# Kernel tuning notes

Hardware: AMD Instinct MI355X
Metric: run time of the kernel (lower is better)

Reference implementation:

```python
import jax, jax.numpy as jnp
import numpy as np

N_NODES = 50000


def gcn_conv(x, W, b, src, dst, n_nodes):
    """PyG GCNConv: h = x @ W; add self-loops; symmetric norm; scatter-add; + bias."""
    h = x @ W  # [N, out]
    loop = jnp.arange(n_nodes, dtype=src.dtype)
    s = jnp.concatenate([src, loop])  # source nodes j
    d = jnp.concatenate([dst, loop])  # target nodes i
    deg = jax.ops.segment_sum(jnp.ones_like(d, dtype=h.dtype), d, num_segments=n_nodes)
    dinv = jnp.where(deg > 0, jax.lax.rsqrt(deg), 0.0)
    norm = dinv[s] * dinv[d]  # [E+N]
    msg = h[s] * norm[:, None]  # gather + scale, [E+N, out]
    out = jax.ops.segment_sum(msg, d, num_segments=n_nodes)
    return out + b


def setup_inputs() -> dict:
    key = jax.random.key(0)
    k1, k2, k3, k4 = jax.random.split(key, 4)
    x = jax.random.normal(k1, (N_NODES, 256), dtype=jnp.float32)
    edge_index = jax.random.randint(k2, (2, 1600000), 0, N_NODES, dtype=jnp.int64)
    in_dim, hid, out_dim = 256, 128, 40
    W1 = jax.random.normal(k3, (in_dim, hid), dtype=jnp.float32) / np.sqrt(in_dim)
    b1 = jnp.zeros((hid,), dtype=jnp.float32)
    W2 = jax.random.normal(k4, (hid, out_dim), dtype=jnp.float32) / np.sqrt(hid)
    b2 = jnp.zeros((out_dim,), dtype=jnp.float32)
    return {"x": x, "edge_index": edge_index, "W1": W1, "b1": b1, "W2": W2, "b2": b2}


def reference(x, edge_index, W1, b1, W2, b2):
    src, dst = edge_index[0], edge_index[1]
    n = x.shape[0]
    h = jax.nn.relu(gcn_conv(x, W1, b1, src, dst, n))
    # dropout is identity in eval mode
    h = gcn_conv(h, W2, b2, src, dst, n)
    return jax.nn.log_softmax(h, axis=1)
```

## Files before the change

kernel.cpp:

```cpp
#include <hip/hip_runtime.h>
#include <cmath>

#define NN 50000
#define C_IN 256
#define C_HID 128
#define C_OUT 40

#define BSZ 512
#define NBUCK ((NN + BSZ - 1) / BSZ)
#define CAP 19456
#define EPB 4096

typedef __attribute__((ext_vector_type(8))) short bf16x8;
typedef __attribute__((ext_vector_type(4))) float f32x4;
typedef __attribute__((ext_vector_type(2))) float f32x2;

__device__ __forceinline__ float bf2f(unsigned int u16) {
  unsigned int b = (u16 & 0xFFFFu) << 16;
  return __builtin_bit_cast(float, b);
}
__device__ __forceinline__ unsigned short f2bf(float f) {
  unsigned int b = __builtin_bit_cast(unsigned int, f);
  unsigned int r = (b + 0x7FFF + ((b >> 16) & 1)) >> 16;
  return (unsigned short)r;
}


__global__ __launch_bounds__(256) void passA_kernel(const int* __restrict__ src,
    const int* __restrict__ dst, int E, unsigned int* __restrict__ gedge,
    int* __restrict__ bcur) {
  __shared__ unsigned int pk[EPB];
  __shared__ unsigned char bof[EPB];
  __shared__ int bcnt[NBUCK], bstart[NBUCK], bpos[NBUCK], gbase[NBUCK];
  int tid = threadIdx.x;
  int e0 = blockIdx.x * EPB;
  int cnt = min(EPB, E - e0);
  for (int b = tid; b < NBUCK; b += 256) bcnt[b] = 0;
  int ds_[16], ss_[16];
  __syncthreads();
  #pragma unroll
  for (int k = 0; k < 16; ++k) {
    int i = tid + k * 256;
    if (i < cnt) {
      ds_[k] = dst[e0 + i];
      ss_[k] = src[e0 + i];
      atomicAdd(&bcnt[ds_[k] >> 9], 1);
    }
  }
  __syncthreads();
  if (tid == 0) {
    int acc = 0;
    for (int b = 0; b < NBUCK; ++b) { bstart[b] = acc; bpos[b] = acc; acc += bcnt[b]; }
  }
  __syncthreads();
  #pragma unroll
  for (int k = 0; k < 16; ++k) {
    int i = tid + k * 256;
    if (i < cnt) {
      int b = ds_[k] >> 9;
      int p = atomicAdd(&bpos[b], 1);
      pk[p] = ((unsigned int)ss_[k] << 9) | (unsigned int)(ds_[k] & 511);
      bof[p] = (unsigned char)b;
    }
  }
  __syncthreads();
  for (int b = tid; b < NBUCK; b += 256)
    gbase[b] = atomicAdd(&bcur[b], bcnt[b]);
  __syncthreads();
  for (int i = tid; i < cnt; i += 256) {
    int b = bof[i];
    int p = gbase[b] + (i - bstart[b]);
    gedge[(size_t)b * CAP + p] = pk[i];
  }
}

__global__ __launch_bounds__(512) void passB_kernel(const unsigned int* __restrict__ gedge,
    const int* __restrict__ bcur, int* __restrict__ esrc, int* __restrict__ off,
    float* __restrict__ dinv, int E) {
  __shared__ int dcnt[512];
  __shared__ int dsc[512];
  __shared__ int dcur[512];
  __shared__ int bc[128];
  int b = blockIdx.x, tid = threadIdx.x;
  int nE = bcur[b];
  if (tid < 128) bc[tid] = (tid < b) ? bcur[tid] : 0;
  dcnt[tid] = 0;
  __syncthreads();
  const unsigned int* reg = gedge + (size_t)b * CAP;
  for (int i = tid; i < nE; i += 512)
    atomicAdd(&dcnt[reg[i] & 511], 1);
  __syncthreads();
  for (int d = 64; d > 0; d >>= 1) {
    if (tid < d) bc[tid] += bc[tid + d];
    __syncthreads();
  }
  int base = bc[0];
  int own = dcnt[tid];
  dsc[tid] = own;
  __syncthreads();
  for (int d = 1; d < 512; d <<= 1) {
    int x = (tid >= d) ? dsc[tid - d] : 0;
    __syncthreads();
    dsc[tid] += x;
    __syncthreads();
  }
  int excl = dsc[tid] - own;
  dcur[tid] = excl;
  int node = b * BSZ + tid;
  if (node < NN) {
    off[node]  = base + excl;
    dinv[node] = rsqrtf((float)(own + 1));
  }
  if (b == 0 && tid == 0) off[NN] = E;
  __syncthreads();
  for (int i = tid; i < nE; i += 512) {
    unsigned int p = reg[i];
    int pos = atomicAdd(&dcur[p & 511], 1);
    esrc[base + pos] = (int)(p >> 9);
  }
}


__global__ void wprep_kernel(const float* __restrict__ W1, const float* __restrict__ W2,
                             const float* __restrict__ b1, uint4* __restrict__ pbuf1,
                             uint4* __restrict__ pbuf2, float* __restrict__ bperm,
                             int* __restrict__ bcur) {
  int blk = blockIdx.x;
  int tid = threadIdx.x;
  if (blk < 16) {
    int gid = blk * 256 + tid;
    int l = gid & 63, idx = gid >> 6;
    int ks = idx & 7, t = idx >> 3;
    int c = t * 16 + (l & 15);
    int kbase = ks * 32 + (l >> 4) * 8;
    unsigned int u[4];
    #pragma unroll
    for (int jp = 0; jp < 4; ++jp) {
      float v0 = W1[(size_t)(kbase + 2 * jp) * C_HID + c];
      float v1 = W1[(size_t)(kbase + 2 * jp + 1) * C_HID + c];
      u[jp] = (unsigned int)f2bf(v0) | ((unsigned int)f2bf(v1) << 16);
    }
    pbuf1[idx * 64 + l] = make_uint4(u[0], u[1], u[2], u[3]);
  } else if (blk < 19) {
    int gid = (blk - 16) * 256 + tid;
    int l = gid & 63, idx = gid >> 6;
    int ks = idx & 3, t = idx >> 2;
    int c = t * 16 + (l & 15);
    int kbase = ks * 32 + (l >> 4) * 8;
    unsigned int u[4];
    #pragma unroll
    for (int jp = 0; jp < 4; ++jp) {
      int k0 = kbase + 2 * jp, k1 = k0 + 1;
      int ch0 = ((k0 & 7) << 4) + (k0 >> 3);
      int ch1 = ((k1 & 7) << 4) + (k1 >> 3);
      float v0 = (c < C_OUT) ? W2[(size_t)ch0 * C_OUT + c] : 0.f;
      float v1 = (c < C_OUT) ? W2[(size_t)ch1 * C_OUT + c] : 0.f;
      u[jp] = (unsigned int)f2bf(v0) | ((unsigned int)f2bf(v1) << 16);
    }
    pbuf2[idx * 64 + l] = make_uint4(u[0], u[1], u[2], u[3]);
  } else {
    if (tid < NBUCK) bcur[tid] = 0;
    if (tid >= 128 && tid < 128 + C_HID) {
      int p = tid - 128;
      bperm[p] = b1[((p & 7) << 4) + (p >> 3)];
    }
  }
}


__global__ __launch_bounds__(256) void gemm1_epack_kernel(const float* __restrict__ x,
    const uint4* __restrict__ pb, uint2* __restrict__ h,
    const int* __restrict__ esrc, const float* __restrict__ dinv,
    unsigned int* __restrict__ epack, int E, int ngemm) {
  if ((int)blockIdx.x >= ngemm) {
    int nb = gridDim.x - ngemm;
    for (int e = (blockIdx.x - ngemm) * 256 + threadIdx.x; e < E; e += nb * 256) {
      int s = esrc[e];
      epack[e] = ((unsigned int)s << 16) | (unsigned int)f2bf(dinv[s]);
    }
    return;
  }
  int l = threadIdx.x & 63, w = threadIdx.x >> 6;
  int row0 = blockIdx.x * 64 + w * 16;
  int arow = min(row0 + (l & 15), NN - 1);
  const float* xp = x + (size_t)arow * C_IN + (l >> 4) * 8;
  bf16x8 a[8];
  #pragma unroll
  for (int ks = 0; ks < 8; ++ks) {
    float4 a0 = *(const float4*)(xp + ks * 32);
    float4 a1 = *(const float4*)(xp + ks * 32 + 4);
    union { bf16x8 v; unsigned short s[8]; } pa;
    pa.s[0] = f2bf(a0.x); pa.s[1] = f2bf(a0.y); pa.s[2] = f2bf(a0.z); pa.s[3] = f2bf(a0.w);
    pa.s[4] = f2bf(a1.x); pa.s[5] = f2bf(a1.y); pa.s[6] = f2bf(a1.z); pa.s[7] = f2bf(a1.w);
    a[ks] = pa.v;
  }
  f32x4 acc[8] = {};
  #pragma unroll
  for (int t = 0; t < 8; ++t) {
    #pragma unroll
    for (int ks = 0; ks < 8; ++ks) {
      bf16x8 b = __builtin_bit_cast(bf16x8, pb[(t * 8 + ks) * 64 + l]);
      acc[t] = __builtin_amdgcn_mfma_f32_16x16x32_bf16(a[ks], b, acc[t], 0, 0, 0);
    }
  }
  int c0 = l & 15, rb = (l >> 4) * 4;
  #pragma unroll
  for (int r = 0; r < 4; ++r) {
    int row = row0 + rb + r;
    if (row < NN) {
      int w0 = __builtin_amdgcn_cvt_pk_fp8_f32(acc[0][r], acc[1][r], 0, false);
      w0     = __builtin_amdgcn_cvt_pk_fp8_f32(acc[2][r], acc[3][r], w0, true);
      int w1 = __builtin_amdgcn_cvt_pk_fp8_f32(acc[4][r], acc[5][r], 0, false);
      w1     = __builtin_amdgcn_cvt_pk_fp8_f32(acc[6][r], acc[7][r], w1, true);
      h[(size_t)row * 16 + c0] = make_uint2((unsigned int)w0, (unsigned int)w1);
    }
  }
}


__global__ __launch_bounds__(256) void gemm2_kernel(const unsigned short* __restrict__ ag1b,
    const uint4* __restrict__ pbuf, unsigned char* __restrict__ h2) {
  int l = threadIdx.x & 63, w = threadIdx.x >> 6;
  int row0 = blockIdx.x * 64 + w * 16;
  int arow = min(row0 + (l & 15), NN - 1);
  const uint4* ap = (const uint4*)(ag1b + (size_t)arow * C_HID + (l >> 4) * 8);
  bf16x8 a[4];
  #pragma unroll
  for (int ks = 0; ks < 4; ++ks) a[ks] = __builtin_bit_cast(bf16x8, ap[ks * 4]);
  f32x4 acc[3] = {};
  #pragma unroll
  for (int t = 0; t < 3; ++t) {
    #pragma unroll
    for (int ks = 0; ks < 4; ++ks) {
      bf16x8 b = __builtin_bit_cast(bf16x8, pbuf[(t * 4 + ks) * 64 + l]);
      acc[t] = __builtin_amdgcn_mfma_f32_16x16x32_bf16(a[ks], b, acc[t], 0, 0, 0);
    }
  }
  int rbase = row0 + (l >> 4) * 4;
  int c0 = l & 15;
  #pragma unroll
  for (int t = 0; t < 3; ++t) {
    int col = t * 16 + c0;
    if (col < C_OUT) {
      #pragma unroll
      for (int r = 0; r < 4; ++r) {
        int row = rbase + r;
        if (row < NN) {
          int pk = __builtin_amdgcn_cvt_pk_fp8_f32(acc[t][r], 0.f, 0, false);
          h2[(size_t)row * C_OUT + col] = (unsigned char)(pk & 0xFF);
        }
      }
    }
  }
}


__global__ void agg1_kernel(const uint2* __restrict__ h, const int* __restrict__ off,
                            const unsigned int* __restrict__ epack,
                            const float* __restrict__ dinv, const float* __restrict__ bperm,
                            uint4* __restrict__ outb, int n, int E) {
  int wv = threadIdx.x >> 6, l = threadIdx.x & 63;
  int i = blockIdx.x * 4 + wv;
  if (i >= n) return;
  int g = l >> 4, q = l & 15;
  float di = dinv[i];
  float a0 = 0.f, a1 = 0.f, a2 = 0.f, a3 = 0.f, a4 = 0.f, a5 = 0.f, a6 = 0.f, a7 = 0.f;
  int p0 = off[i], p1 = off[i + 1];
  int pb = p0;
  int Em1 = E - 1;
  unsigned int e0 = epack[min(pb + g, Em1)];
  unsigned int e1 = epack[min(pb + 4 + g, Em1)];
  unsigned int e2 = epack[min(pb + 8 + g, Em1)];
  unsigned int e3 = epack[min(pb + 12 + g, Em1)];
  unsigned int f0 = epack[min(pb + 16 + g, Em1)];
  unsigned int f1 = epack[min(pb + 20 + g, Em1)];
  unsigned int f2 = epack[min(pb + 24 + g, Em1)];
  unsigned int f3 = epack[min(pb + 28 + g, Em1)];
  uint2 H0 = h[(size_t)(e0 >> 16) * 16 + q];
  uint2 H1 = h[(size_t)(e1 >> 16) * 16 + q];
  uint2 H2 = h[(size_t)(e2 >> 16) * 16 + q];
  uint2 H3 = h[(size_t)(e3 >> 16) * 16 + q];
  #define ACC_EDGE(vv, ee)                                                    \
    {                                                                         \
      float n_ = bf2f(ee) * di;                                               \
      f32x2 c0_ = __builtin_amdgcn_cvt_pk_f32_fp8((int)vv.x, false);          \
      f32x2 c1_ = __builtin_amdgcn_cvt_pk_f32_fp8((int)vv.x, true);           \
      f32x2 c2_ = __builtin_amdgcn_cvt_pk_f32_fp8((int)vv.y, false);          \
      f32x2 c3_ = __builtin_amdgcn_cvt_pk_f32_fp8((int)vv.y, true);           \
      a0 += c0_[0] * n_; a1 += c0_[1] * n_;                                   \
      a2 += c1_[0] * n_; a3 += c1_[1] * n_;                                   \
      a4 += c2_[0] * n_; a5 += c2_[1] * n_;                                   \
      a6 += c3_[0] * n_; a7 += c3_[1] * n_;                                   \
    }
  for (; pb + 31 < p1; pb += 16) {
    uint2 G0 = h[(size_t)(f0 >> 16) * 16 + q];
    uint2 G1 = h[(size_t)(f1 >> 16) * 16 + q];
    uint2 G2 = h[(size_t)(f2 >> 16) * 16 + q];
    uint2 G3 = h[(size_t)(f3 >> 16) * 16 + q];
    unsigned int n0 = epack[min(pb + 32 + g, Em1)];
    unsigned int n1 = epack[min(pb + 36 + g, Em1)];
    unsigned int n2 = epack[min(pb + 40 + g, Em1)];
    unsigned int n3 = epack[min(pb + 44 + g, Em1)];
    ACC_EDGE(H0, e0); ACC_EDGE(H1, e1); ACC_EDGE(H2, e2); ACC_EDGE(H3, e3);
    e0 = f0; e1 = f1; e2 = f2; e3 = f3;
    f0 = n0; f1 = n1; f2 = n2; f3 = n3;
    H0 = G0; H1 = G1; H2 = G2; H3 = G3;
  }
  if (pb + g < p1)      ACC_EDGE(H0, e0);
  if (pb + 4 + g < p1)  ACC_EDGE(H1, e1);
  if (pb + 8 + g < p1)  ACC_EDGE(H2, e2);
  if (pb + 12 + g < p1) ACC_EDGE(H3, e3);
  int pc = pb + 16;
  if (pc < p1) {
    uint2 G0 = h[(size_t)(f0 >> 16) * 16 + q];
    uint2 G1 = h[(size_t)(f1 >> 16) * 16 + q];
    uint2 G2 = h[(size_t)(f2 >> 16) * 16 + q];
    uint2 G3 = h[(size_t)(f3 >> 16) * 16 + q];
    if (pc + g < p1)      ACC_EDGE(G0, f0);
    if (pc + 4 + g < p1)  ACC_EDGE(G1, f1);
    if (pc + 8 + g < p1)  ACC_EDGE(G2, f2);
    if (pc + 12 + g < p1) ACC_EDGE(G3, f3);
  }
  #undef ACC_EDGE
  a0 += __shfl_xor(a0, 16); a1 += __shfl_xor(a1, 16);
  a2 += __shfl_xor(a2, 16); a3 += __shfl_xor(a3, 16);
  a4 += __shfl_xor(a4, 16); a5 += __shfl_xor(a5, 16);
  a6 += __shfl_xor(a6, 16); a7 += __shfl_xor(a7, 16);
  a0 += __shfl_xor(a0, 32); a1 += __shfl_xor(a1, 32);
  a2 += __shfl_xor(a2, 32); a3 += __shfl_xor(a3, 32);
  a4 += __shfl_xor(a4, 32); a5 += __shfl_xor(a5, 32);
  a6 += __shfl_xor(a6, 32); a7 += __shfl_xor(a7, 32);
  if (g == 0) {
    uint2 sv = h[(size_t)i * 16 + q];
    float dd = di * di;
    f32x2 s0 = __builtin_amdgcn_cvt_pk_f32_fp8((int)sv.x, false);
    f32x2 s1 = __builtin_amdgcn_cvt_pk_f32_fp8((int)sv.x, true);
    f32x2 s2 = __builtin_amdgcn_cvt_pk_f32_fp8((int)sv.y, false);
    f32x2 s3 = __builtin_amdgcn_cvt_pk_f32_fp8((int)sv.y, true);
    a0 += s0[0] * dd; a1 += s0[1] * dd;
    a2 += s1[0] * dd; a3 += s1[1] * dd;
    a4 += s2[0] * dd; a5 += s2[1] * dd;
    a6 += s3[0] * dd; a7 += s3[1] * dd;
    float4 b0 = ((const float4*)bperm)[q * 2];
    float4 b1v = ((const float4*)bperm)[q * 2 + 1];
    a0 = fmaxf(a0 + b0.x, 0.f); a1 = fmaxf(a1 + b0.y, 0.f);
    a2 = fmaxf(a2 + b0.z, 0.f); a3 = fmaxf(a3 + b0.w, 0.f);
    a4 = fmaxf(a4 + b1v.x, 0.f); a5 = fmaxf(a5 + b1v.y, 0.f);
    a6 = fmaxf(a6 + b1v.z, 0.f); a7 = fmaxf(a7 + b1v.w, 0.f);
    uint4 o;
    o.x = (unsigned int)f2bf(a0) | ((unsigned int)f2bf(a1) << 16);
    o.y = (unsigned int)f2bf(a2) | ((unsigned int)f2bf(a3) << 16);
    o.z = (unsigned int)f2bf(a4) | ((unsigned int)f2bf(a5) << 16);
    o.w = (unsigned int)f2bf(a6) | ((unsigned int)f2bf(a7) << 16);
    outb[(size_t)i * 16 + q] = o;
  }
}

__global__ void agg2_kernel(const unsigned char* __restrict__ h2, const int* __restrict__ off,
                            const unsigned int* __restrict__ epack,
                            const float* __restrict__ dinv, const float* __restrict__ b,
                            float* __restrict__ out, int n, int E) {
  int wv = threadIdx.x >> 6, l = threadIdx.x & 63;
  int i = blockIdx.x * 4 + wv;
  if (i >= n) return;
  int g = l / 10, q = l - g * 10;
  bool lact = l < 60;
  if (!lact) { g = 0; q = 0; }
  float di = dinv[i];
  float a0 = 0.f, a1 = 0.f, a2 = 0.f, a3 = 0.f;
  int p0 = off[i], p1 = off[i + 1];
  int pb = p0;
  int Em1 = E - 1;
  unsigned int e0 = epack[min(pb + g, Em1)];
  unsigned int e1 = epack[min(pb + 6 + g, Em1)];
  unsigned int f0 = epack[min(pb + 12 + g, Em1)];
  unsigned int f1 = epack[min(pb + 18 + g, Em1)];
  unsigned int H0 = *(const unsigned int*)(h2 + (size_t)(e0 >> 16) * C_OUT + q * 4);
  unsigned int H1 = *(const unsigned int*)(h2 + (size_t)(e1 >> 16) * C_OUT + q * 4);
  #define ACC_EDGE2(vv, ee)                                                   \
    {                                                                         \
      float n_ = bf2f(ee) * di;                                               \
      f32x2 lo_ = __builtin_amdgcn_cvt_pk_f32_fp8((int)(vv), false);          \
      f32x2 hi_ = __builtin_amdgcn_cvt_pk_f32_fp8((int)(vv), true);           \
      a0 += lo_[0] * n_; a1 += lo_[1] * n_;                                   \
      a2 += hi_[0] * n_; a3 += hi_[1] * n_;                                   \
    }
  for (; pb + 23 < p1; pb += 12) {
    unsigned int G0 = *(const unsigned int*)(h2 + (size_t)(f0 >> 16) * C_OUT + q * 4);
    unsigned int G1 = *(const unsigned int*)(h2 + (size_t)(f1 >> 16) * C_OUT + q * 4);
    unsigned int n0 = epack[min(pb + 24 + g, Em1)];
    unsigned int n1 = epack[min(pb + 30 + g, Em1)];
    if (lact) { ACC_EDGE2(H0, e0); ACC_EDGE2(H1, e1); }
    e0 = f0; e1 = f1;
    f0 = n0; f1 = n1;
    H0 = G0; H1 = G1;
  }
  if (lact && pb + g < p1)     ACC_EDGE2(H0, e0);
  if (lact && pb + 6 + g < p1) ACC_EDGE2(H1, e1);
  int pc = pb + 12;
  if (pc < p1) {
    unsigned int G0 = *(const unsigned int*)(h2 + (size_t)(f0 >> 16) * C_OUT + q * 4);
    unsigned int G1 = *(const unsigned int*)(h2 + (size_t)(f1 >> 16) * C_OUT + q * 4);
    if (lact && pc + g < p1)     ACC_EDGE2(G0, f0);
    if (lact && pc + 6 + g < p1) ACC_EDGE2(G1, f1);
  }
  #undef ACC_EDGE2
  float t0 = 0.f, t1 = 0.f, t2 = 0.f, t3 = 0.f;
  #pragma unroll
  for (int gg = 0; gg < 6; ++gg) {
    int sl = gg * 10 + q;
    t0 += __shfl(a0, sl); t1 += __shfl(a1, sl);
    t2 += __shfl(a2, sl); t3 += __shfl(a3, sl);
  }
  bool act = l < 10;
  float v0, v1, v2, v3;
  if (act) {
    unsigned int sv = *(const unsigned int*)(h2 + (size_t)i * C_OUT + l * 4);
    f32x2 slo = __builtin_amdgcn_cvt_pk_f32_fp8((int)sv, false);
    f32x2 shi = __builtin_amdgcn_cvt_pk_f32_fp8((int)sv, true);
    float dd = di * di;
    float4 bb = ((const float4*)b)[l];
    v0 = t0 + slo[0] * dd + bb.x;
    v1 = t1 + slo[1] * dd + bb.y;
    v2 = t2 + shi[0] * dd + bb.z;
    v3 = t3 + shi[1] * dd + bb.w;
  } else {
    v0 = v1 = v2 = v3 = -INFINITY;
  }
  float mm = fmaxf(fmaxf(v0, v1), fmaxf(v2, v3));
  #pragma unroll
  for (int d = 32; d > 0; d >>= 1) mm = fmaxf(mm, __shfl_xor(mm, d));
  float e = act ? (expf(v0 - mm) + expf(v1 - mm) + expf(v2 - mm) + expf(v3 - mm)) : 0.f;
  float ss = e;
  #pragma unroll
  for (int d = 32; d > 0; d >>= 1) ss += __shfl_xor(ss, d);
  if (act) {
    float lg = logf(ss);
    float4 o = {v0 - mm - lg, v1 - mm - lg, v2 - mm - lg, v3 - mm - lg};
    *(float4*)&out[(size_t)i * C_OUT + l * 4] = o;
  }
}


extern "C" void kernel_launch(void* const* d_in, const int* in_sizes, int n_in,
                              void* d_out, int out_size, void* d_ws, size_t ws_size,
                              hipStream_t stream) {
  const float* x  = (const float*)d_in[0];
  const int*   ei = (const int*)d_in[1];
  const float* W1 = (const float*)d_in[2];
  const float* b1 = (const float*)d_in[3];
  const float* W2 = (const float*)d_in[4];
  const float* b2 = (const float*)d_in[5];
  int E = in_sizes[1] / 2;
  const int* src = ei;
  const int* dst = ei + E;

  char* ws = (char*)d_ws;
  size_t o = 0;
  auto alloc = [&](size_t bytes) {
    char* p = ws + o;
    o += (bytes + 255) & ~(size_t)255;
    return p;
  };
  unsigned int* gedge = (unsigned int*)alloc((size_t)NBUCK * CAP * sizeof(unsigned int));
  int*   bcur  = (int*)alloc(NBUCK * sizeof(int));
  int*   off   = (int*)alloc((NN + 1) * sizeof(int));
  float* dinv  = (float*)alloc(NN * sizeof(float));
  int*   esrc  = (int*)alloc((size_t)E * sizeof(int));
  unsigned int* epack = (unsigned int*)alloc((size_t)E * sizeof(unsigned int));
  uint2* h1f8  = (uint2*)alloc((size_t)NN * C_HID);
  unsigned int*   ag1b = (unsigned int*)alloc((size_t)NN * (C_HID / 2) * sizeof(unsigned int));
  unsigned char*  h2f8 = (unsigned char*)alloc((size_t)NN * C_OUT);
  uint4* pbuf2 = (uint4*)alloc(12 * 64 * sizeof(uint4));
  uint4* pbuf1 = (uint4*)alloc(64 * 64 * sizeof(uint4));
  float* bperm = (float*)alloc(C_HID * sizeof(float));

  int ngemm = (NN + 63) / 64;

  wprep_kernel<<<20, 256, 0, stream>>>(W1, W2, b1, pbuf1, pbuf2, bperm, bcur);
  passA_kernel<<<(E + EPB - 1) / EPB, 256, 0, stream>>>(src, dst, E, gedge, bcur);
  passB_kernel<<<NBUCK, 512, 0, stream>>>(gedge, bcur, esrc, off, dinv, E);
  gemm1_epack_kernel<<<ngemm + 512, 256, 0, stream>>>(x, pbuf1, h1f8, esrc, dinv,
                                                      epack, E, ngemm);
  agg1_kernel<<<(NN + 3) / 4, 256, 0, stream>>>(h1f8, off, epack, dinv, bperm,
                                                (uint4*)ag1b, NN, E);
  gemm2_kernel<<<ngemm, 256, 0, stream>>>((const unsigned short*)ag1b, pbuf2, h2f8);
  agg2_kernel<<<(NN + 3) / 4, 256, 0, stream>>>(h2f8, off, epack, dinv, b2,
                                                (float*)d_out, NN, E);
}
```

Baseline: 135.1 us.

## Fuse GEMM1 with edge bucketing and build packed edge records in passB

Merges the first dense GEMM into the edge bucketing kernel as extra blocks, so the two run concurrently inside one launch. Per-node in-degrees are counted with global atomics during bucketing. passB then writes the packed (src, dinv) edge records directly, which removes the separate esrc array and the epack pass that reread it. The cost is 1.6M extra global atomics on the count array and another zeroing range in wprep, and passB now does a random read of cnt[s] for every edge.

After: 197.0 us. 1.46x slower.

```diff
diff --git a/kernel.cpp b/kernel.cpp
--- a/kernel.cpp
+++ b/kernel.cpp
@@ -26,25 +26,116 @@
 }
 
 
-__global__ __launch_bounds__(256) void passA_kernel(const int* __restrict__ src,
-    const int* __restrict__ dst, int E, unsigned int* __restrict__ gedge,
-    int* __restrict__ bcur) {
+__global__ void wprep_kernel(const float* __restrict__ W1, const float* __restrict__ W2,
+                             const float* __restrict__ b1, uint4* __restrict__ pbuf1,
+                             uint4* __restrict__ pbuf2, float* __restrict__ bperm,
+                             int* __restrict__ bcur, int* __restrict__ cnt) {
+  int blk = blockIdx.x;
+  int tid = threadIdx.x;
+  if (blk < 16) {
+    int gid = blk * 256 + tid;
+    int l = gid & 63, idx = gid >> 6;
+    int ks = idx & 7, t = idx >> 3;
+    int c = t * 16 + (l & 15);
+    int kbase = ks * 32 + (l >> 4) * 8;
+    unsigned int u[4];
+    #pragma unroll
+    for (int jp = 0; jp < 4; ++jp) {
+      float v0 = W1[(size_t)(kbase + 2 * jp) * C_HID + c];
+      float v1 = W1[(size_t)(kbase + 2 * jp + 1) * C_HID + c];
+      u[jp] = (unsigned int)f2bf(v0) | ((unsigned int)f2bf(v1) << 16);
+    }
+    pbuf1[idx * 64 + l] = make_uint4(u[0], u[1], u[2], u[3]);
+  } else if (blk < 19) {
+    int gid = (blk - 16) * 256 + tid;
+    int l = gid & 63, idx = gid >> 6;
+    int ks = idx & 3, t = idx >> 2;
+    int c = t * 16 + (l & 15);
+    int kbase = ks * 32 + (l >> 4) * 8;
+    unsigned int u[4];
+    #pragma unroll
+    for (int jp = 0; jp < 4; ++jp) {
+      int k0 = kbase + 2 * jp, k1 = k0 + 1;
+      int ch0 = ((k0 & 7) << 4) + (k0 >> 3);
+      int ch1 = ((k1 & 7) << 4) + (k1 >> 3);
+      float v0 = (c < C_OUT) ? W2[(size_t)ch0 * C_OUT + c] : 0.f;
+      float v1 = (c < C_OUT) ? W2[(size_t)ch1 * C_OUT + c] : 0.f;
+      u[jp] = (unsigned int)f2bf(v0) | ((unsigned int)f2bf(v1) << 16);
+    }
+    pbuf2[idx * 64 + l] = make_uint4(u[0], u[1], u[2], u[3]);
+  } else if (blk == 19) {
+    if (tid < NBUCK) bcur[tid] = 0;
+    if (tid >= 128 && tid < 128 + C_HID) {
+      int p = tid - 128;
+      bperm[p] = b1[((p & 7) << 4) + (p >> 3)];
+    }
+  } else {
+    int i = (blk - 20) * 256 + tid;
+    if (i < NN) cnt[i] = 0;
+  }
+}
+
+
+__global__ __launch_bounds__(256) void g1passA_kernel(const float* __restrict__ x,
+    const uint4* __restrict__ pb, uint2* __restrict__ h,
+    const int* __restrict__ src, const int* __restrict__ dst, int E,
+    unsigned int* __restrict__ gedge, int* __restrict__ bcur, int* __restrict__ cnt,
+    int ngemm) {
   __shared__ unsigned int pk[EPB];
   __shared__ unsigned char bof[EPB];
   __shared__ int bcnt[NBUCK], bstart[NBUCK], bpos[NBUCK], gbase[NBUCK];
   int tid = threadIdx.x;
-  int e0 = blockIdx.x * EPB;
-  int cnt = min(EPB, E - e0);
+  if ((int)blockIdx.x < ngemm) {
+    int l = tid & 63, w = tid >> 6;
+    int row0 = blockIdx.x * 64 + w * 16;
+    int arow = min(row0 + (l & 15), NN - 1);
+    const float* xp = x + (size_t)arow * C_IN + (l >> 4) * 8;
+    bf16x8 a[8];
+    #pragma unroll
+    for (int ks = 0; ks < 8; ++ks) {
+      float4 a0 = *(const float4*)(xp + ks * 32);
+      float4 a1 = *(const float4*)(xp + ks * 32 + 4);
+      union { bf16x8 v; unsigned short s[8]; } pa;
+      pa.s[0] = f2bf(a0.x); pa.s[1] = f2bf(a0.y); pa.s[2] = f2bf(a0.z); pa.s[3] = f2bf(a0.w);
+      pa.s[4] = f2bf(a1.x); pa.s[5] = f2bf(a1.y); pa.s[6] = f2bf(a1.z); pa.s[7] = f2bf(a1.w);
+      a[ks] = pa.v;
+    }
+    f32x4 acc[8] = {};
+    #pragma unroll
+    for (int t = 0; t < 8; ++t) {
+      #pragma unroll
+      for (int ks = 0; ks < 8; ++ks) {
+        bf16x8 b = __builtin_bit_cast(bf16x8, pb[(t * 8 + ks) * 64 + l]);
+        acc[t] = __builtin_amdgcn_mfma_f32_16x16x32_bf16(a[ks], b, acc[t], 0, 0, 0);
+      }
+    }
+    int c0 = l & 15, rb = (l >> 4) * 4;
+    #pragma unroll
+    for (int r = 0; r < 4; ++r) {
+      int row = row0 + rb + r;
+      if (row < NN) {
+        int w0 = __builtin_amdgcn_cvt_pk_fp8_f32(acc[0][r], acc[1][r], 0, false);
+        w0     = __builtin_amdgcn_cvt_pk_fp8_f32(acc[2][r], acc[3][r], w0, true);
+        int w1 = __builtin_amdgcn_cvt_pk_fp8_f32(acc[4][r], acc[5][r], 0, false);
+        w1     = __builtin_amdgcn_cvt_pk_fp8_f32(acc[6][r], acc[7][r], w1, true);
+        h[(size_t)row * 16 + c0] = make_uint2((unsigned int)w0, (unsigned int)w1);
+      }
+    }
+    return;
+  }
+  int e0 = (blockIdx.x - ngemm) * EPB;
+  int cntE = min(EPB, E - e0);
   for (int b = tid; b < NBUCK; b += 256) bcnt[b] = 0;
   int ds_[16], ss_[16];
   __syncthreads();
   #pragma unroll
   for (int k = 0; k < 16; ++k) {
     int i = tid + k * 256;
-    if (i < cnt) {
+    if (i < cntE) {
       ds_[k] = dst[e0 + i];
       ss_[k] = src[e0 + i];
       atomicAdd(&bcnt[ds_[k] >> 9], 1);
+      atomicAdd(&cnt[ds_[k]], 1);
     }
   }
   __syncthreads();
@@ -56,7 +147,7 @@
   #pragma unroll
   for (int k = 0; k < 16; ++k) {
     int i = tid + k * 256;
-    if (i < cnt) {
+    if (i < cntE) {
       int b = ds_[k] >> 9;
       int p = atomicAdd(&bpos[b], 1);
       pk[p] = ((unsigned int)ss_[k] << 9) | (unsigned int)(ds_[k] & 511);
@@ -67,15 +158,17 @@
   for (int b = tid; b < NBUCK; b += 256)
     gbase[b] = atomicAdd(&bcur[b], bcnt[b]);
   __syncthreads();
-  for (int i = tid; i < cnt; i += 256) {
+  for (int i = tid; i < cntE; i += 256) {
     int b = bof[i];
     int p = gbase[b] + (i - bstart[b]);
     gedge[(size_t)b * CAP + p] = pk[i];
   }
 }
 
+
 __global__ __launch_bounds__(512) void passB_kernel(const unsigned int* __restrict__ gedge,
-    const int* __restrict__ bcur, int* __restrict__ esrc, int* __restrict__ off,
+    const int* __restrict__ bcur, const int* __restrict__ cnt,
+    unsigned int* __restrict__ epck, int* __restrict__ off,
     float* __restrict__ dinv, int E) {
   __shared__ int dcnt[512];
   __shared__ int dsc[512];
@@ -115,105 +208,10 @@
   __syncthreads();
   for (int i = tid; i < nE; i += 512) {
     unsigned int p = reg[i];
+    int s = (int)(p >> 9);
     int pos = atomicAdd(&dcur[p & 511], 1);
-    esrc[base + pos] = (int)(p >> 9);
-  }
-}
-
-
-__global__ void wprep_kernel(const float* __restrict__ W1, const float* __restrict__ W2,
-                             const float* __restrict__ b1, uint4* __restrict__ pbuf1,
-                             uint4* __restrict__ pbuf2, float* __restrict__ bperm,
-                             int* __restrict__ bcur) {
-  int blk = blockIdx.x;
-  int tid = threadIdx.x;
-  if (blk < 16) {
-    int gid = blk * 256 + tid;
-    int l = gid & 63, idx = gid >> 6;
-    int ks = idx & 7, t = idx >> 3;
-    int c = t * 16 + (l & 15);
-    int kbase = ks * 32 + (l >> 4) * 8;
-    unsigned int u[4];
-    #pragma unroll
-    for (int jp = 0; jp < 4; ++jp) {
-      float v0 = W1[(size_t)(kbase + 2 * jp) * C_HID + c];
-      float v1 = W1[(size_t)(kbase + 2 * jp + 1) * C_HID + c];
-      u[jp] = (unsigned int)f2bf(v0) | ((unsigned int)f2bf(v1) << 16);
-    }
-    pbuf1[idx * 64 + l] = make_uint4(u[0], u[1], u[2], u[3]);
-  } else if (blk < 19) {
-    int gid = (blk - 16) * 256 + tid;
-    int l = gid & 63, idx = gid >> 6;
-    int ks = idx & 3, t = idx >> 2;
-    int c = t * 16 + (l & 15);
-    int kbase = ks * 32 + (l >> 4) * 8;
-    unsigned int u[4];
-    #pragma unroll
-    for (int jp = 0; jp < 4; ++jp) {
-      int k0 = kbase + 2 * jp, k1 = k0 + 1;
-      int ch0 = ((k0 & 7) << 4) + (k0 >> 3);
-      int ch1 = ((k1 & 7) << 4) + (k1 >> 3);
-      float v0 = (c < C_OUT) ? W2[(size_t)ch0 * C_OUT + c] : 0.f;
-      float v1 = (c < C_OUT) ? W2[(size_t)ch1 * C_OUT + c] : 0.f;
-      u[jp] = (unsigned int)f2bf(v0) | ((unsigned int)f2bf(v1) << 16);
-    }
-    pbuf2[idx * 64 + l] = make_uint4(u[0], u[1], u[2], u[3]);
-  } else {
-    if (tid < NBUCK) bcur[tid] = 0;
-    if (tid >= 128 && tid < 128 + C_HID) {
-      int p = tid - 128;
-      bperm[p] = b1[((p & 7) << 4) + (p >> 3)];
-    }
-  }
-}
-
-
-__global__ __launch_bounds__(256) void gemm1_epack_kernel(const float* __restrict__ x,
-    const uint4* __restrict__ pb, uint2* __restrict__ h,
-    const int* __restrict__ esrc, const float* __restrict__ dinv,
-    unsigned int* __restrict__ epack, int E, int ngemm) {
-  if ((int)blockIdx.x >= ngemm) {
-    int nb = gridDim.x - ngemm;
-    for (int e = (blockIdx.x - ngemm) * 256 + threadIdx.x; e < E; e += nb * 256) {
-      int s = esrc[e];
-      epack[e] = ((unsigned int)s << 16) | (unsigned int)f2bf(dinv[s]);
-    }
-    return;
-  }
-  int l = threadIdx.x & 63, w = threadIdx.x >> 6;
-  int row0 = blockIdx.x * 64 + w * 16;
-  int arow = min(row0 + (l & 15), NN - 1);
-  const float* xp = x + (size_t)arow * C_IN + (l >> 4) * 8;
-  bf16x8 a[8];
-  #pragma unroll
-  for (int ks = 0; ks < 8; ++ks) {
-    float4 a0 = *(const float4*)(xp + ks * 32);
-    float4 a1 = *(const float4*)(xp + ks * 32 + 4);
-    union { bf16x8 v; unsigned short s[8]; } pa;
-    pa.s[0] = f2bf(a0.x); pa.s[1] = f2bf(a0.y); pa.s[2] = f2bf(a0.z); pa.s[3] = f2bf(a0.w);
-    pa.s[4] = f2bf(a1.x); pa.s[5] = f2bf(a1.y); pa.s[6] = f2bf(a1.z); pa.s[7] = f2bf(a1.w);
-    a[ks] = pa.v;
-  }
-  f32x4 acc[8] = {};
-  #pragma unroll
-  for (int t = 0; t < 8; ++t) {
-    #pragma unroll
-    for (int ks = 0; ks < 8; ++ks) {
-      bf16x8 b = __builtin_bit_cast(bf16x8, pb[(t * 8 + ks) * 64 + l]);
-      acc[t] = __builtin_amdgcn_mfma_f32_16x16x32_bf16(a[ks], b, acc[t], 0, 0, 0);
-    }
-  }
-  int c0 = l & 15, rb = (l >> 4) * 4;
-  #pragma unroll
-  for (int r = 0; r < 4; ++r) {
-    int row = row0 + rb + r;
-    if (row < NN) {
-      int w0 = __builtin_amdgcn_cvt_pk_fp8_f32(acc[0][r], acc[1][r], 0, false);
-      w0     = __builtin_amdgcn_cvt_pk_fp8_f32(acc[2][r], acc[3][r], w0, true);
-      int w1 = __builtin_amdgcn_cvt_pk_fp8_f32(acc[4][r], acc[5][r], 0, false);
-      w1     = __builtin_amdgcn_cvt_pk_fp8_f32(acc[6][r], acc[7][r], w1, true);
-      h[(size_t)row * 16 + c0] = make_uint2((unsigned int)w0, (unsigned int)w1);
-    }
+    float dv = rsqrtf((float)(cnt[s] + 1));
+    epck[base + pos] = ((unsigned int)s << 16) | (unsigned int)f2bf(dv);
   }
 }
 
@@ -464,10 +462,10 @@
   };
   unsigned int* gedge = (unsigned int*)alloc((size_t)NBUCK * CAP * sizeof(unsigned int));
   int*   bcur  = (int*)alloc(NBUCK * sizeof(int));
+  int*   cnt   = (int*)alloc(NN * sizeof(int));
   int*   off   = (int*)alloc((NN + 1) * sizeof(int));
   float* dinv  = (float*)alloc(NN * sizeof(float));
-  int*   esrc  = (int*)alloc((size_t)E * sizeof(int));
-  unsigned int* epack = (unsigned int*)alloc((size_t)E * sizeof(unsigned int));
+  unsigned int* epck = (unsigned int*)alloc((size_t)E * sizeof(unsigned int));
   uint2* h1f8  = (uint2*)alloc((size_t)NN * C_HID);
   unsigned int*   ag1b = (unsigned int*)alloc((size_t)NN * (C_HID / 2) * sizeof(unsigned int));
   unsigned char*  h2f8 = (unsigned char*)alloc((size_t)NN * C_OUT);
@@ -476,15 +474,16 @@
   float* bperm = (float*)alloc(C_HID * sizeof(float));
 
   int ngemm = (NN + 63) / 64;
-
-  wprep_kernel<<<20, 256, 0, stream>>>(W1, W2, b1, pbuf1, pbuf2, bperm, bcur);
-  passA_kernel<<<(E + EPB - 1) / EPB, 256, 0, stream>>>(src, dst, E, gedge, bcur);
-  passB_kernel<<<NBUCK, 512, 0, stream>>>(gedge, bcur, esrc, off, dinv, E);
-  gemm1_epack_kernel<<<ngemm + 512, 256, 0, stream>>>(x, pbuf1, h1f8, esrc, dinv,
-                                                      epack, E, ngemm);
-  agg1_kernel<<<(NN + 3) / 4, 256, 0, stream>>>(h1f8, off, epack, dinv, bperm,
+  int nA = (E + EPB - 1) / EPB;
+  int nzero = (NN + 255) / 256;
+
+  wprep_kernel<<<20 + nzero, 256, 0, stream>>>(W1, W2, b1, pbuf1, pbuf2, bperm, bcur, cnt);
+  g1passA_kernel<<<ngemm + nA, 256, 0, stream>>>(x, pbuf1, h1f8, src, dst, E,
+                                                 gedge, bcur, cnt, ngemm);
+  passB_kernel<<<NBUCK, 512, 0, stream>>>(gedge, bcur, cnt, epck, off, dinv, E);
+  agg1_kernel<<<(NN + 3) / 4, 256, 0, stream>>>(h1f8, off, epck, dinv, bperm,
                                                 (uint4*)ag1b, NN, E);
   gemm2_kernel<<<ngemm, 256, 0, stream>>>((const unsigned short*)ag1b, pbuf2, h2f8);
-  agg2_kernel<<<(NN + 3) / 4, 256, 0, stream>>>(h2f8, off, epack, dinv, b2,
+  agg2_kernel<<<(NN + 3) / 4, 256, 0, stream>>>(h2f8, off, epck, dinv, b2,
                                                 (float*)d_out, NN, E);
 }
```
